# Performance work log

Hardware: AMD Instinct MI355X
Metric: run time of the kernel (lower is better)

## Reference

```python
import jax, jax.numpy as jnp
import numpy as np

N0, N1, N2 = 80000, 40000, 20000
E1, E2 = 500000, 250000
FIN = 128        # in_channels
H = 2            # heads
C1 = 64          # hidden_channels -> layer1 out per head (concat -> 128)
C2 = 64          # out_channels -> layer2 out per head (mean over heads)
ED = 10          # edge_dim per embedding, total edge feat = 2*ED = 20
NTYPE, NTS = 23, 1158


def setup_inputs() -> dict:
    key = jax.random.key(0)
    ks = jax.random.split(key, 48)
    sc = 0.05
    inp = {
        "x": jax.random.normal(ks[0], (N0, FIN), jnp.float32),
        "ei1_src": jax.random.randint(ks[1], (E1,), 0, N0),
        "ei1_dst": jax.random.randint(ks[2], (E1,), 0, N1),
        "et1": jax.random.randint(ks[3], (E1,), 0, NTYPE),
        "ets1": jax.random.randint(ks[4], (E1,), 0, NTS),
        "ei2_src": jax.random.randint(ks[5], (E2,), 0, N1),
        "ei2_dst": jax.random.randint(ks[6], (E2,), 0, N2),
        "et2": jax.random.randint(ks[7], (E2,), 0, NTYPE),
        "ets2": jax.random.randint(ks[8], (E2,), 0, NTS),
        # shared edge embeddings (Linear(23,10), Linear(1158,10))
        "edge_W": jax.random.normal(ks[9], (ED, NTYPE), jnp.float32) * sc,
        "edge_b": jax.random.normal(ks[10], (ED,), jnp.float32) * sc,
        "time_W": jax.random.normal(ks[11], (ED, NTS), jnp.float32) * sc,
        "time_b": jax.random.normal(ks[12], (ED,), jnp.float32) * sc,
    }
    # layer 1: in=128, heads=2, C=64, concat=True (out dim 128)
    hc1 = H * C1
    inp["Wq1"] = jax.random.normal(ks[13], (hc1, FIN), jnp.float32) * sc
    inp["bq1"] = jnp.zeros((hc1,), jnp.float32)
    inp["Wk1"] = jax.random.normal(ks[14], (hc1, FIN), jnp.float32) * sc
    inp["bk1"] = jnp.zeros((hc1,), jnp.float32)
    inp["Wv1"] = jax.random.normal(ks[15], (hc1, FIN), jnp.float32) * sc
    inp["bv1"] = jnp.zeros((hc1,), jnp.float32)
    inp["We1"] = jax.random.normal(ks[16], (hc1, 2 * ED), jnp.float32) * sc
    inp["Wskip1"] = jax.random.normal(ks[17], (hc1, FIN), jnp.float32) * sc
    inp["bskip1"] = jnp.zeros((hc1,), jnp.float32)
    inp["Wbeta1"] = jax.random.normal(ks[18], (1, 3 * hc1), jnp.float32) * sc
    inp["ln_g"] = jnp.ones((hc1,), jnp.float32)
    inp["ln_b"] = jnp.zeros((hc1,), jnp.float32)
    # layer 2: in=128, heads=2, C=64, concat=False (out dim 64)
    hc2 = H * C2
    inp["Wq2"] = jax.random.normal(ks[19], (hc2, hc1), jnp.float32) * sc
    inp["bq2"] = jnp.zeros((hc2,), jnp.float32)
    inp["Wk2"] = jax.random.normal(ks[20], (hc2, hc1), jnp.float32) * sc
    inp["bk2"] = jnp.zeros((hc2,), jnp.float32)
    inp["Wv2"] = jax.random.normal(ks[21], (hc2, hc1), jnp.float32) * sc
    inp["bv2"] = jnp.zeros((hc2,), jnp.float32)
    inp["We2"] = jax.random.normal(ks[22], (hc2, 2 * ED), jnp.float32) * sc
    inp["Wskip2"] = jax.random.normal(ks[23], (C2, hc1), jnp.float32) * sc
    inp["bskip2"] = jnp.zeros((C2,), jnp.float32)
    inp["Wbeta2"] = jax.random.normal(ks[24], (1, 3 * C2), jnp.float32) * sc
    return inp


def _edge_feat(et, ets, edge_W, edge_b, time_W, time_b):
    # one_hot(e) @ W.T + b == W.T[e] + b (avoids materializing huge one-hot)
    return jnp.concatenate([jnp.take(edge_W.T, et, axis=0) + edge_b,
                            jnp.take(time_W.T, ets, axis=0) + time_b], axis=-1)


def _conv(x_src, x_dst, src, dst, ef, Wq, bq, Wk, bk, Wv, bv, We,
          Wskip, bskip, Wbeta, concat):
    n_dst = x_dst.shape[0]
    HC = Wq.shape[0]
    C = HC // H
    q = (x_dst @ Wq.T + bq).reshape(n_dst, H, C)            # [Nd,H,C]
    k = (x_src @ Wk.T + bk)[src].reshape(-1, H, C)          # [E,H,C]
    v = (x_src @ Wv.T + bv)[src].reshape(-1, H, C)
    e = (ef @ We.T).reshape(-1, H, C)
    k = k + e
    alpha = jnp.einsum('ehc,ehc->eh', q[dst], k) / np.sqrt(C).astype(np.float32)
    # segment softmax over destination nodes
    m = jax.ops.segment_max(alpha, dst, num_segments=n_dst)
    ex = jnp.exp(alpha - m[dst])
    s = jax.ops.segment_sum(ex, dst, num_segments=n_dst)
    a = ex / (s[dst] + 1e-16)                               # [E,H]
    msg = (v + e) * a[..., None]                            # [E,H,C]
    out = jax.ops.segment_sum(msg.reshape(-1, HC), dst, num_segments=n_dst)
    out = out if concat else out.reshape(n_dst, H, C).mean(axis=1)
    x_r = x_dst @ Wskip.T + bskip
    beta = jax.nn.sigmoid(
        jnp.concatenate([out, x_r, out - x_r], axis=-1) @ Wbeta.T)  # [Nd,1]
    return beta * x_r + (1.0 - beta) * out


def _layernorm(x, g, b):
    mu = x.mean(-1, keepdims=True)
    var = x.var(-1, keepdims=True)
    return (x - mu) / jnp.sqrt(var + 1e-5) * g + b


def reference(x, ei1_src, ei1_dst, et1, ets1, ei2_src, ei2_dst, et2, ets2,
              edge_W, edge_b, time_W, time_b,
              Wq1, bq1, Wk1, bk1, Wv1, bv1, We1, Wskip1, bskip1, Wbeta1,
              ln_g, ln_b,
              Wq2, bq2, Wk2, bk2, Wv2, bv2, We2, Wskip2, bskip2, Wbeta2):
    ef1 = _edge_feat(et1, ets1, edge_W, edge_b, time_W, time_b)
    h = _conv(x, x[:N1], ei1_src, ei1_dst, ef1,
              Wq1, bq1, Wk1, bk1, Wv1, bv1, We1, Wskip1, bskip1, Wbeta1,
              concat=True)
    h = jax.nn.gelu(_layernorm(h, ln_g, ln_b), approximate=False)
    ef2 = _edge_feat(et2, ets2, edge_W, edge_b, time_W, time_b)
    o = _conv(h, h[:N2], ei2_src, ei2_dst, ef2,
              Wq2, bq2, Wk2, bk2, Wv2, bv2, We2, Wskip2, bskip2, Wbeta2,
              concat=False)
    return jax.nn.log_softmax(o, axis=-1)
```

## Files before the change

### kernel.cpp

```cpp
#include <hip/hip_runtime.h>
#include <math.h>

#define N0 80000
#define N1 40000
#define N2 20000
#define E1C 500000
#define E2C 250000
#define NTYPE 23
#define NTS 1158

#define NB1 157
#define NB2 79
#define KV1B 1250
#define QR1B 625
#define CNTB 2930
#define KV2B 625
#define QR2B 313
#define FILLB 2930
#define AGG1B 2048
#define AGG2B 1024

#define OFF_XB    0u
#define OFF_QR1   5120000u
#define OFF_KV1   15360000u
#define OFF_H     25600000u
#define OFF_QR2   28160000u
#define OFF_KV2   32000000u
#define OFF_WB1   37120000u
#define OFF_BP1   37160000u
#define OFF_WB2   37170000u
#define OFF_BP2   37200000u
#define OFF_TA1   37210000u
#define OFF_TB1   37213000u
#define OFF_TA2   37370000u
#define OFF_TB2   37373000u
#define OFF_RP1   37530000u
#define OFF_CUR1  37580000u
#define OFF_ED1   37630000u
#define OFF_BS1   38640000u
#define OFF_RP2   38650000u
#define OFF_CUR2  38680000u
#define OFF_ED2   38710000u
#define OFF_BS2   39220000u
#define OFF_DONE  39230000u
#define OFF_RK1   39240000u
#define OFF_RK2   39740000u

typedef __bf16 bf16x8 __attribute__((ext_vector_type(8)));
typedef float f32x4 __attribute__((ext_vector_type(4)));

static __device__ __forceinline__ float b2f(unsigned short u) {
    union { unsigned int i; float f; } c;
    c.i = ((unsigned int)u) << 16;
    return c.f;
}
static __device__ __forceinline__ unsigned short f2b(float f) {
    unsigned int u = __float_as_uint(f);
    unsigned int r = (u + 0x7fffu + ((u >> 16) & 1u)) >> 16;
    return (unsigned short)r;
}
static __device__ __forceinline__ bf16x8 ldfrag(const unsigned short* p) {
    return *reinterpret_cast<const bf16x8*>(p);
}

static __device__ __forceinline__ void stage16(const void* g, void* l) {
    __builtin_amdgcn_global_load_lds(
        (const __attribute__((address_space(1))) unsigned int*)g,
        (__attribute__((address_space(3))) unsigned int*)l,
        16, 0, 0);
}

template <int CTRL>
static __device__ __forceinline__ float dpp_addstep(float v) {
    int x = __builtin_amdgcn_mov_dpp(__float_as_int(v), CTRL, 0xF, 0xF, true);
    return v + __int_as_float(x);
}
static __device__ __forceinline__ float red16(float v) {
    v = dpp_addstep<0xB1>(v);
    v = dpp_addstep<0x4E>(v);
    v = dpp_addstep<0x141>(v);
    v = dpp_addstep<0x140>(v);
    return v;
}
template <int CTRL>
static __device__ __forceinline__ float dpp_maxstep(float v) {
    int x = __builtin_amdgcn_mov_dpp(__float_as_int(v), CTRL, 0xF, 0xF, true);
    return fmaxf(v, __int_as_float(x));
}
static __device__ __forceinline__ float red16max(float v) {
    v = dpp_maxstep<0xB1>(v);
    v = dpp_maxstep<0x4E>(v);
    v = dpp_maxstep<0x141>(v);
    v = dpp_maxstep<0x140>(v);
    return v;
}

#define LDSS 136
#define SMEM_USHORTS 8704

template <int NTILES>
static __device__ __forceinline__ void dev_gemm_bf16out(
    const unsigned short* __restrict__ XB, const unsigned short* __restrict__ WB,
    const float* __restrict__ BP, unsigned short* __restrict__ Y, int n, int blk,
    unsigned short* sb) {
    constexpr int COLS = NTILES * 16;
    constexpr int HALF = NTILES / 2;
    constexpr int HCOLS = HALF * 16;
    constexpr int NCHUNK = (NTILES + 3) / 4;
    int wave = threadIdx.x >> 6, lane = threadIdx.x & 63;
    int m = lane & 15, quad = lane >> 4;
    int rowbase = blk * 64 + wave * 16;
    int arow = rowbase + m; if (arow >= n) arow = n - 1;
    unsigned short* swave = sb + wave * 16 * LDSS;
    const unsigned short* xrow = XB + (size_t)arow * 128 + quad * 8;
    bf16x8 a0 = ldfrag(xrow), a1 = ldfrag(xrow + 32);
    bf16x8 a2 = ldfrag(xrow + 64), a3 = ldfrag(xrow + 96);
    f32x4 acc[NTILES];
#pragma unroll
    for (int t = 0; t < NTILES; t++) acc[t] = (f32x4){0.f, 0.f, 0.f, 0.f};
    const char* gstage = (const char*)WB + wave * 1024 + lane * 16;
    char* lstage = (char*)sb + wave * 1024;
#pragma unroll
    for (int c = 0; c < NCHUNK; c++) {
#pragma unroll
        for (int i = 0; i < 4; i++)
            if (c * 4 + i < NTILES)
                stage16(gstage + (size_t)(c * 4 + i) * 4096, lstage + i * 4096);
        __syncthreads();
#pragma unroll
        for (int t = 0; t < 4; t++) {
            int tt = c * 4 + t;
            if (tt < NTILES) {
                const unsigned short* wt = sb + t * 2048 + lane * 8;
                acc[tt] = __builtin_amdgcn_mfma_f32_16x16x32_bf16(a0, ldfrag(wt), acc[tt], 0, 0, 0);
                acc[tt] = __builtin_amdgcn_mfma_f32_16x16x32_bf16(a1, ldfrag(wt + 512), acc[tt], 0, 0, 0);
                acc[tt] = __builtin_amdgcn_mfma_f32_16x16x32_bf16(a2, ldfrag(wt + 1024), acc[tt], 0, 0, 0);
                acc[tt] = __builtin_amdgcn_mfma_f32_16x16x32_bf16(a3, ldfrag(wt + 1536), acc[tt], 0, 0, 0);
            }
        }
        __syncthreads();
    }
    int tswz_bit = (quad >> 1) & 1;
#pragma unroll
    for (int half = 0; half < 2; half++) {
#pragma unroll
        for (int t = 0; t < HALF; t++) {
            int tt = half * HALF + t;
            int tsw = t ^ tswz_bit;
            float b = BP[tt * 16 + m];
#pragma unroll
            for (int r = 0; r < 4; r++)
                swave[(quad * 4 + r) * LDSS + tsw * 16 + m] = f2b(acc[tt][r] + b);
        }
#pragma unroll
        for (int i = 0; i < 4; i++) {
            int idx = i * 64 + lane;
            int r = idx / (HCOLS / 8), g = idx % (HCOLS / 8);
            int gs = g ^ (((r >> 3) & 1) << 1);
            int grow = rowbase + r;
            if (grow < n) {
                uint4 v = *(const uint4*)&swave[r * LDSS + gs * 8];
                *(uint4*)(Y + (size_t)grow * COLS + half * HCOLS + g * 8) = v;
            }
        }
    }
}

template <int NTILES>
static __device__ __forceinline__ void dev_gemm_f32out(
    const unsigned short* __restrict__ XB, const unsigned short* __restrict__ WB,
    const float* __restrict__ BP, float* __restrict__ Y, int n, int blk,
    unsigned short* sb) {
    constexpr int COLS = NTILES * 16;
    constexpr int NCHUNK = (NTILES + 3) / 4;
    int wave = threadIdx.x >> 6, lane = threadIdx.x & 63;
    int m = lane & 15, quad = lane >> 4;
    int rowbase = blk * 64 + wave * 16;
    int arow = rowbase + m; if (arow >= n) arow = n - 1;
    const unsigned short* xrow = XB + (size_t)arow * 128 + quad * 8;
    bf16x8 a0 = ldfrag(xrow), a1 = ldfrag(xrow + 32);
    bf16x8 a2 = ldfrag(xrow + 64), a3 = ldfrag(xrow + 96);
    f32x4 acc[NTILES];
#pragma unroll
    for (int t = 0; t < NTILES; t++) acc[t] = (f32x4){0.f, 0.f, 0.f, 0.f};
    const char* gstage = (const char*)WB + wave * 1024 + lane * 16;
    char* lstage = (char*)sb + wave * 1024;
#pragma unroll
    for (int c = 0; c < NCHUNK; c++) {
#pragma unroll
        for (int i = 0; i < 4; i++)
            if (c * 4 + i < NTILES)
                stage16(gstage + (size_t)(c * 4 + i) * 4096, lstage + i * 4096);
        __syncthreads();
#pragma unroll
        for (int t = 0; t < 4; t++) {
            int tt = c * 4 + t;
            if (tt < NTILES) {
                const unsigned short* wt = sb + t * 2048 + lane * 8;
                acc[tt] = __builtin_amdgcn_mfma_f32_16x16x32_bf16(a0, ldfrag(wt), acc[tt], 0, 0, 0);
                acc[tt] = __builtin_amdgcn_mfma_f32_16x16x32_bf16(a1, ldfrag(wt + 512), acc[tt], 0, 0, 0);
                acc[tt] = __builtin_amdgcn_mfma_f32_16x16x32_bf16(a2, ldfrag(wt + 1024), acc[tt], 0, 0, 0);
                acc[tt] = __builtin_amdgcn_mfma_f32_16x16x32_bf16(a3, ldfrag(wt + 1536), acc[tt], 0, 0, 0);
            }
        }
        __syncthreads();
    }
#pragma unroll
    for (int t = 0; t < NTILES; t++) {
        float b = BP[t * 16 + m];
#pragma unroll
        for (int r = 0; r < 4; r++) {
            int grow = rowbase + quad * 4 + r;
            if (grow < n) Y[(size_t)grow * COLS + t * 16 + m] = acc[t][r] + b;
        }
    }
}

__global__ __launch_bounds__(256) void prep(
    const float* __restrict__ x, unsigned short* __restrict__ XB,
    const float* __restrict__ Wk1, const float* __restrict__ Wv1,
    const float* __restrict__ Wq1, const float* __restrict__ Wskip1,
    const float* __restrict__ bk1, const float* __restrict__ bv1,
    const float* __restrict__ bq1, const float* __restrict__ bskip1,
    const float* __restrict__ Wk2, const float* __restrict__ Wv2,
    const float* __restrict__ Wq2, const float* __restrict__ Wskip2,
    const float* __restrict__ bk2, const float* __restrict__ bv2,
    const float* __restrict__ bq2, const float* __restrict__ bskip2,
    unsigned short* __restrict__ WB1, float* __restrict__ BP1,
    unsigned short* __restrict__ WB2, float* __restrict__ BP2,
    const float* __restrict__ edge_W, const float* __restrict__ edge_b,
    const float* __restrict__ time_W, const float* __restrict__ time_b,
    const float* __restrict__ We1, const float* __restrict__ We2,
    float* __restrict__ TA1, float* __restrict__ TB1,
    float* __restrict__ TA2, float* __restrict__ TB2,
    int* __restrict__ cnt1, int* __restrict__ cnt2, int* __restrict__ done) {
    int tid = blockIdx.x * blockDim.x + threadIdx.x;
    int stride = gridDim.x * blockDim.x;
    for (int i = tid; i < N0 * 32; i += stride) {
        float4 v = *(const float4*)(x + (size_t)i * 4);
        ushort4 u;
        u.x = f2b(v.x); u.y = f2b(v.y); u.z = f2b(v.z); u.w = f2b(v.w);
        *(ushort4*)(XB + (size_t)i * 4) = u;
    }
    for (int i = tid; i < 512 * 128; i += stride) {
        int j = i & 7, l = (i >> 3) & 63, ks = (i >> 9) & 3, t = i >> 11;
        int row = t * 16 + (l & 15);
        int col = ks * 32 + ((l >> 4) & 3) * 8 + j;
        const float* w; int off;
        if (row < 128) { w = Wk1; off = 0; }
        else if (row < 256) { w = Wv1; off = 128; }
        else if (row < 384) { w = Wq1; off = 256; }
        else { w = Wskip1; off = 384; }
        WB1[i] = f2b(w[(size_t)(row - off) * 128 + col]);
    }
    for (int i = tid; i < 512; i += stride) {
        const float* b; int off;
        if (i < 128) { b = bk1; off = 0; }
        else if (i < 256) { b = bv1; off = 128; }
        else if (i < 384) { b = bq1; off = 256; }
        else { b = bskip1; off = 384; }
        BP1[i] = b[i - off];
    }
    for (int i = tid; i < 448 * 128; i += stride) {
        int j = i & 7, l = (i >> 3) & 63, ks = (i >> 9) & 3, t = i >> 11;
        int row = t * 16 + (l & 15);
        int col = ks * 32 + ((l >> 4) & 3) * 8 + j;
        const float* w; int off;
        if (row < 128) { w = Wk2; off = 0; }
        else if (row < 256) { w = Wv2; off = 128; }
        else if (row < 384) { w = Wq2; off = 256; }
        else { w = Wskip2; off = 384; }
        WB2[i] = f2b(w[(size_t)(row - off) * 128 + col]);
    }
    for (int i = tid; i < 448; i += stride) {
        const float* b; int off;
        if (i < 128) { b = bk2; off = 0; }
        else if (i < 256) { b = bv2; off = 128; }
        else if (i < 384) { b = bq2; off = 256; }
        else { b = bskip2; off = 384; }
        BP2[i] = b[i - off];
    }
    const int TBL = (NTYPE + NTS) * 128;
    for (int i = tid; i < TBL; i += stride) {
        if (i < NTYPE * 128) {
            int e = i >> 7, c = i & 127;
            float s1 = 0.f, s2 = 0.f;
#pragma unroll
            for (int j = 0; j < 10; j++) {
                float fj = edge_W[j * NTYPE + e] + edge_b[j];
                s1 += fj * We1[c * 20 + j];
                s2 += fj * We2[c * 20 + j];
            }
            TA1[i] = s1; TA2[i] = s2;
        } else {
            int u = i - NTYPE * 128;
            int ts = u >> 7, c = u & 127;
            float s1 = 0.f, s2 = 0.f;
#pragma unroll
            for (int j = 0; j < 10; j++) {
                float fj = time_W[j * NTS + ts] + time_b[j];
                s1 += fj * We1[c * 20 + 10 + j];
                s2 += fj * We2[c * 20 + 10 + j];
            }
            TB1[u] = s1; TB2[u] = s2;
        }
    }
    for (int i = tid; i < N1 + N2 + 2; i += stride) {
        if (i < N1) cnt1[i] = 0;
        else if (i < N1 + N2) cnt2[i - N1] = 0;
        else done[i - N1 - N2] = 0;
    }
}

__global__ __launch_bounds__(256) void mega_l1(
    const unsigned short* __restrict__ XB,
    const unsigned short* __restrict__ WB1, const float* __restrict__ BP1,
    unsigned short* __restrict__ KV1, float* __restrict__ QR1,
    const int* __restrict__ d1, const int* __restrict__ d2,
    int* __restrict__ cnt1, int* __restrict__ cnt2,
    int* __restrict__ rk1, int* __restrict__ rk2) {
    __shared__ __align__(16) unsigned short sbuf[SMEM_USHORTS];
    int b = blockIdx.x;
    if (b < CNTB) {
        int t = b * 256 + threadIdx.x;
        if (t < E1C) rk1[t] = atomicAdd(&cnt1[d1[t]], 1);
        else {
            t -= E1C;
            if (t < E2C) rk2[t] = atomicAdd(&cnt2[d2[t]], 1);
        }
    } else if (b < CNTB + KV1B) {
        dev_gemm_bf16out<16>(XB, WB1, BP1, KV1, N0, b - CNTB, sbuf);
    } else {
        dev_gemm_f32out<16>(XB, WB1 + 256 * 128, BP1 + 256, QR1, N1,
                            b - CNTB - KV1B, sbuf);
    }
}

__global__ __launch_bounds__(256) void gemm_l2(
    const unsigned short* __restrict__ H,
    const unsigned short* __restrict__ WB2, const float* __restrict__ BP2,
    unsigned short* __restrict__ KV2, float* __restrict__ QR2) {
    __shared__ __align__(16) unsigned short sbuf[SMEM_USHORTS];
    int b = blockIdx.x;
    if (b < KV2B) dev_gemm_bf16out<16>(H, WB2, BP2, KV2, N1, b, sbuf);
    else dev_gemm_f32out<12>(H, WB2 + 256 * 128, BP2 + 256, QR2, N2, b - KV2B, sbuf);
}

__global__ __launch_bounds__(256) void csr_scan(
    int* __restrict__ cnt1, int* __restrict__ bs1, int* __restrict__ rp1,
    int* __restrict__ cnt2, int* __restrict__ bs2, int* __restrict__ rp2,
    int* __restrict__ done) {
    __shared__ int s[256];
    __shared__ int amlast;
    int b = blockIdx.x;
    int* cnt; int* bs; int* rp; int n, lb;
    if (b < NB1) { cnt = cnt1; bs = bs1; rp = rp1; n = N1; lb = b; }
    else { cnt = cnt2; bs = bs2; rp = rp2; n = N2; lb = b - NB1; }
    int t = lb * 256 + threadIdx.x;
    int v = (t < n) ? cnt[t] : 0;
    s[threadIdx.x] = v;
    __syncthreads();
    for (int off = 128; off; off >>= 1) {
        if (threadIdx.x < off) s[threadIdx.x] += s[threadIdx.x + off];
        __syncthreads();
    }
    if (threadIdx.x == 0) {
        atomicExch(&bs[lb], s[0]);
        __threadfence();
        int prev = atomicAdd(&done[0], 1);
        amlast = (prev == NB1 + NB2 - 1) ? 1 : 0;
    }
    __syncthreads();
    if (amlast) {
        int tt = threadIdx.x;
        int v1 = (tt < NB1) ? atomicAdd(&bs1[tt], 0) : 0;
        s[tt] = v1;
        __syncthreads();
        for (int off = 1; off < 256; off <<= 1) {
            int u = (tt >= off) ? s[tt - off] : 0;
            __syncthreads();
            s[tt] += u;
            __syncthreads();
        }
        if (tt < NB1) atomicExch(&bs1[tt], s[tt] - v1);
        __syncthreads();
        int v2 = (tt < NB2) ? atomicAdd(&bs2[tt], 0) : 0;
        s[tt] = v2;
        __syncthreads();
        for (int off = 1; off < 256; off <<= 1) {
            int u = (tt >= off) ? s[tt - off] : 0;
            __syncthreads();
            s[tt] += u;
            __syncthreads();
        }
        if (tt < NB2) atomicExch(&bs2[tt], s[tt] - v2);
        __threadfence();
        __syncthreads();
        if (tt == 0) atomicExch(&done[1], 1);
    }
    if (threadIdx.x == 0) {
        while (atomicAdd(&done[1], 0) == 0) __builtin_amdgcn_s_sleep(1);
    }
    __syncthreads();
    __threadfence();
    int base = atomicAdd(&bs[lb], 0);
    s[threadIdx.x] = v;
    __syncthreads();
    for (int off = 1; off < 256; off <<= 1) {
        int u = (threadIdx.x >= off) ? s[threadIdx.x - off] : 0;
        __syncthreads();
        s[threadIdx.x] += u;
        __syncthreads();
    }
    int incl = s[threadIdx.x];
    if (t < n) rp[t] = base + incl - v;
    if (t == n - 1) rp[n] = base + incl;
}

__global__ __launch_bounds__(256) void fill_both(
    const int* __restrict__ d1, const int* __restrict__ s1,
    const int* __restrict__ et1, const int* __restrict__ ets1,
    const int* __restrict__ rp1, const int* __restrict__ rk1, uint2* __restrict__ ed1,
    const int* __restrict__ d2, const int* __restrict__ s2,
    const int* __restrict__ et2, const int* __restrict__ ets2,
    const int* __restrict__ rp2, const int* __restrict__ rk2, uint2* __restrict__ ed2) {
    int t = blockIdx.x * 256 + threadIdx.x;
    if (t < E1C) {
        int pos = rp1[d1[t]] + rk1[t];
        ed1[pos] = make_uint2((unsigned)s1[t],
                              (unsigned)(et1[t] | (ets1[t] << 16)));
    } else {
        t -= E1C;
        if (t < E2C) {
            int pos = rp2[d2[t]] + rk2[t];
            ed2[pos] = make_uint2((unsigned)s2[t],
                                  (unsigned)(et2[t] | (ets2[t] << 16)));
        }
    }
}

static __device__ __forceinline__ void edge_accum(
    int beg, int end, int s, int co, float4 q4,
    const uint2* __restrict__ ED, const float* __restrict__ TA,
    const float* __restrict__ TB, const unsigned short* __restrict__ KV,
    float& ax, float& ay, float& az, float& aw, float& suma) {
    int p = beg + s;
    if (p >= end) return;
    uint2 d0 = ED[p];
    int pA = p + 2;  bool mA = pA < end;
    uint2 d1 = ED[mA ? pA : beg];
    int pB = p + 4;  bool mB = pB < end;
    uint2 d2 = ED[mB ? pB : beg];
    int sn0 = (int)d0.x, t0 = (int)(d0.y & 0xFFFF), ts0 = (int)(d0.y >> 16);
    float4 ta0 = *(const float4*)(TA + t0 * 128 + co);
    float4 tb0 = *(const float4*)(TB + ts0 * 128 + co);
    const unsigned short* kv0 = KV + (size_t)sn0 * 256;
    ushort4 ku0 = *(const ushort4*)(kv0 + co);
    ushort4 vu0 = *(const ushort4*)(kv0 + 128 + co);
    int sn1 = (int)d1.x, t1 = (int)(d1.y & 0xFFFF), ts1 = (int)(d1.y >> 16);
    float4 ta1 = *(const float4*)(TA + t1 * 128 + co);
    float4 tb1 = *(const float4*)(TB + ts1 * 128 + co);
    const unsigned short* kv1 = KV + (size_t)sn1 * 256;
    ushort4 ku1 = *(const ushort4*)(kv1 + co);
    ushort4 vu1 = *(const ushort4*)(kv1 + 128 + co);
    for (;;) {
        int pC = pB + 2; bool mC = pC < end;
        uint2 d3 = ED[mC ? pC : beg];
        int sn2 = (int)d2.x, t2 = (int)(d2.y & 0xFFFF), ts2 = (int)(d2.y >> 16);
        float4 ta2 = *(const float4*)(TA + t2 * 128 + co);
        float4 tb2 = *(const float4*)(TB + ts2 * 128 + co);
        const unsigned short* kv2 = KV + (size_t)sn2 * 256;
        ushort4 ku2 = *(const ushort4*)(kv2 + co);
        ushort4 vu2 = *(const ushort4*)(kv2 + 128 + co);
        float e0c = ta0.x + tb0.x, e1c = ta0.y + tb0.y;
        float e2c = ta0.z + tb0.z, e3c = ta0.w + tb0.w;
        float pp = q4.x * (b2f(ku0.x) + e0c) + q4.y * (b2f(ku0.y) + e1c)
                 + q4.z * (b2f(ku0.z) + e2c) + q4.w * (b2f(ku0.w) + e3c);
        pp = red16(pp);
        float a = __expf(pp * 0.125f);
        ax += a * (b2f(vu0.x) + e0c); ay += a * (b2f(vu0.y) + e1c);
        az += a * (b2f(vu0.z) + e2c); aw += a * (b2f(vu0.w) + e3c);
        suma += a;
        if (!mA) break;
        ta0 = ta1; tb0 = tb1; ku0 = ku1; vu0 = vu1;
        ta1 = ta2; tb1 = tb2; ku1 = ku2; vu1 = vu2;
        d2 = d3;
        mA = mB; mB = mC; pB = pC;
    }
}

__global__ __launch_bounds__(256) void agg_layer1(
    const int* __restrict__ rowptr, const uint2* __restrict__ ED,
    const float* __restrict__ TA, const float* __restrict__ TB,
    const float* __restrict__ QR, const unsigned short* __restrict__ KV,
    const float* __restrict__ Wbeta,
    const float* __restrict__ ln_g, const float* __restrict__ ln_b,
    unsigned short* __restrict__ hout, int n) {
    int gw = (blockIdx.x * blockDim.x + threadIdx.x) >> 6;
    int nw = (gridDim.x * blockDim.x) >> 6;
    int lane = threadIdx.x & 63;
    int s = lane >> 5, cg = lane & 15;
    int co = ((lane >> 4) & 1) * 64 + 4 * cg;
    for (int wid = gw; wid < n; wid += nw) {
    int beg = rowptr[wid], end = rowptr[wid + 1];
    float4 q4 = *(const float4*)(QR + (size_t)wid * 256 + co);
    float ax = 0.f, ay = 0.f, az = 0.f, aw = 0.f, suma = 0.f;
    edge_accum(beg, end, s, co, q4, ED, TA, TB, KV, ax, ay, az, aw, suma);
    ax += __shfl_xor(ax, 32); ay += __shfl_xor(ay, 32);
    az += __shfl_xor(az, 32); aw += __shfl_xor(aw, 32);
    suma += __shfl_xor(suma, 32);
    float inv_s = 1.f / (suma + 1e-16f);
    float ox = ax * inv_s, oy = ay * inv_s, oz = az * inv_s, ow = aw * inv_s;
    float4 r4 = *(const float4*)(QR + (size_t)wid * 256 + 128 + co);
    float4 wo = *(const float4*)(Wbeta + co);
    float4 wr = *(const float4*)(Wbeta + 128 + co);
    float4 wd = *(const float4*)(Wbeta + 256 + co);
    float pb = wo.x * ox + wr.x * r4.x + wd.x * (ox - r4.x)
             + wo.y * oy + wr.y * r4.y + wd.y * (oy - r4.y)
             + wo.z * oz + wr.z * r4.z + wd.z * (oz - r4.z)
             + wo.w * ow + wr.w * r4.w + wd.w * (ow - r4.w);
    pb = red16(pb);
    pb += __shfl_xor(pb, 16);
    float beta = 1.f / (1.f + __expf(-pb));
    float gx = beta * r4.x + (1.f - beta) * ox;
    float gy = beta * r4.y + (1.f - beta) * oy;
    float gz = beta * r4.z + (1.f - beta) * oz;
    float gw4 = beta * r4.w + (1.f - beta) * ow;
    float sm = gx + gy + gz + gw4;
    float sq = gx * gx + gy * gy + gz * gz + gw4 * gw4;
    sm = red16(sm); sm += __shfl_xor(sm, 16);
    sq = red16(sq); sq += __shfl_xor(sq, 16);
    float mu = sm * (1.f / 128.f);
    float var = sq * (1.f / 128.f) - mu * mu;
    float inv = rsqrtf(var + 1e-5f);
    float4 lg = *(const float4*)(ln_g + co);
    float4 lb = *(const float4*)(ln_b + co);
    float yx = (gx - mu) * inv * lg.x + lb.x;
    float yy = (gy - mu) * inv * lg.y + lb.y;
    float yz = (gz - mu) * inv * lg.z + lb.z;
    float yw = (gw4 - mu) * inv * lg.w + lb.w;
    const float ISQ2 = 0.70710678118654752f;
    yx = 0.5f * yx * (1.f + erff(yx * ISQ2));
    yy = 0.5f * yy * (1.f + erff(yy * ISQ2));
    yz = 0.5f * yz * (1.f + erff(yz * ISQ2));
    yw = 0.5f * yw * (1.f + erff(yw * ISQ2));
    if (s == 0) {
        ushort4 hv;
        hv.x = f2b(yx); hv.y = f2b(yy); hv.z = f2b(yz); hv.w = f2b(yw);
        *(ushort4*)(hout + (size_t)wid * 128 + co) = hv;
    }
    }
}

__global__ __launch_bounds__(256) void agg_layer2(
    const int* __restrict__ rowptr, const uint2* __restrict__ ED,
    const float* __restrict__ TA, const float* __restrict__ TB,
    const float* __restrict__ QR, const unsigned short* __restrict__ KV,
    const float* __restrict__ Wbeta,
    float* __restrict__ o, int n) {
    int gw = (blockIdx.x * blockDim.x + threadIdx.x) >> 6;
    int nw = (gridDim.x * blockDim.x) >> 6;
    int lane = threadIdx.x & 63;
    int s = lane >> 5, cg = lane & 15;
    int co = ((lane >> 4) & 1) * 64 + 4 * cg;
    for (int wid = gw; wid < n; wid += nw) {
    int beg = rowptr[wid], end = rowptr[wid + 1];
    float4 q4 = *(const float4*)(QR + (size_t)wid * 192 + co);
    float ax = 0.f, ay = 0.f, az = 0.f, aw = 0.f, suma = 0.f;
    edge_accum(beg, end, s, co, q4, ED, TA, TB, KV, ax, ay, az, aw, suma);
    ax += __shfl_xor(ax, 32); ay += __shfl_xor(ay, 32);
    az += __shfl_xor(az, 32); aw += __shfl_xor(aw, 32);
    suma += __shfl_xor(suma, 32);
    float inv_s = 1.f / (suma + 1e-16f);
    float ox = ax * inv_s, oy = ay * inv_s, oz = az * inv_s, ow = aw * inv_s;
    ox = 0.5f * (ox + __shfl_xor(ox, 16));
    oy = 0.5f * (oy + __shfl_xor(oy, 16));
    oz = 0.5f * (oz + __shfl_xor(oz, 16));
    ow = 0.5f * (ow + __shfl_xor(ow, 16));
    float4 r4 = *(const float4*)(QR + (size_t)wid * 192 + 128 + 4 * cg);
    float4 wo = *(const float4*)(Wbeta + 4 * cg);
    float4 wr = *(const float4*)(Wbeta + 64 + 4 * cg);
    float4 wd = *(const float4*)(Wbeta + 128 + 4 * cg);
    float pb = wo.x * ox + wr.x * r4.x + wd.x * (ox - r4.x)
             + wo.y * oy + wr.y * r4.y + wd.y * (oy - r4.y)
             + wo.z * oz + wr.z * r4.z + wd.z * (oz - r4.z)
             + wo.w * ow + wr.w * r4.w + wd.w * (ow - r4.w);
    pb = red16(pb);
    float beta = 1.f / (1.f + __expf(-pb));
    float vx = beta * r4.x + (1.f - beta) * ox;
    float vy = beta * r4.y + (1.f - beta) * oy;
    float vz = beta * r4.z + (1.f - beta) * oz;
    float vw = beta * r4.w + (1.f - beta) * ow;
    float m = fmaxf(fmaxf(vx, vy), fmaxf(vz, vw));
    m = red16max(m);
    float se = __expf(vx - m) + __expf(vy - m) + __expf(vz - m) + __expf(vw - m);
    se = red16(se);
    float lse = m + logf(se);
    if (lane < 16)
        *(float4*)(o + (size_t)wid * 64 + 4 * cg) =
            make_float4(vx - lse, vy - lse, vz - lse, vw - lse);
    }
}

extern "C" void kernel_launch(void* const* d_in, const int* in_sizes, int n_in,
                              void* d_out, int out_size, void* d_ws, size_t ws_size,
                              hipStream_t stream) {
    const float* x        = (const float*)d_in[0];
    const int*   ei1_src  = (const int*)d_in[1];
    const int*   ei1_dst  = (const int*)d_in[2];
    const int*   et1      = (const int*)d_in[3];
    const int*   ets1     = (const int*)d_in[4];
    const int*   ei2_src  = (const int*)d_in[5];
    const int*   ei2_dst  = (const int*)d_in[6];
    const int*   et2      = (const int*)d_in[7];
    const int*   ets2     = (const int*)d_in[8];
    const float* edge_W   = (const float*)d_in[9];
    const float* edge_b   = (const float*)d_in[10];
    const float* time_W   = (const float*)d_in[11];
    const float* time_b   = (const float*)d_in[12];
    const float* Wq1      = (const float*)d_in[13];
    const float* bq1      = (const float*)d_in[14];
    const float* Wk1      = (const float*)d_in[15];
    const float* bk1      = (const float*)d_in[16];
    const float* Wv1      = (const float*)d_in[17];
    const float* bv1      = (const float*)d_in[18];
    const float* We1      = (const float*)d_in[19];
    const float* Wskip1   = (const float*)d_in[20];
    const float* bskip1   = (const float*)d_in[21];
    const float* Wbeta1   = (const float*)d_in[22];
    const float* ln_g     = (const float*)d_in[23];
    const float* ln_b     = (const float*)d_in[24];
    const float* Wq2      = (const float*)d_in[25];
    const float* bq2      = (const float*)d_in[26];
    const float* Wk2      = (const float*)d_in[27];
    const float* bk2      = (const float*)d_in[28];
    const float* Wv2      = (const float*)d_in[29];
    const float* bv2      = (const float*)d_in[30];
    const float* We2      = (const float*)d_in[31];
    const float* Wskip2   = (const float*)d_in[32];
    const float* bskip2   = (const float*)d_in[33];
    const float* Wbeta2   = (const float*)d_in[34];

    float* ws = (float*)d_ws;
    unsigned short* xb  = (unsigned short*)(ws + OFF_XB);
    float* qr1          = ws + OFF_QR1;
    unsigned short* kv1 = (unsigned short*)(ws + OFF_KV1);
    unsigned short* h   = (unsigned short*)(ws + OFF_H);
    float* qr2          = ws + OFF_QR2;
    unsigned short* kv2 = (unsigned short*)(ws + OFF_KV2);
    unsigned short* wb1 = (unsigned short*)(ws + OFF_WB1);
    float* bp1          = ws + OFF_BP1;
    unsigned short* wb2 = (unsigned short*)(ws + OFF_WB2);
    float* bp2          = ws + OFF_BP2;
    float* ta1          = ws + OFF_TA1;
    float* tb1          = ws + OFF_TB1;
    float* ta2          = ws + OFF_TA2;
    float* tb2          = ws + OFF_TB2;
    int*   rp1          = (int*)(ws + OFF_RP1);
    int*   cur1         = (int*)(ws + OFF_CUR1);
    uint2* ed1          = (uint2*)(ws + OFF_ED1);
    int*   bs1          = (int*)(ws + OFF_BS1);
    int*   rp2          = (int*)(ws + OFF_RP2);
    int*   cur2         = (int*)(ws + OFF_CUR2);
    uint2* ed2          = (uint2*)(ws + OFF_ED2);
    int*   bs2          = (int*)(ws + OFF_BS2);
    int*   done         = (int*)(ws + OFF_DONE);
    int*   rk1          = (int*)(ws + OFF_RK1);
    int*   rk2          = (int*)(ws + OFF_RK2);

    prep<<<2048, 256, 0, stream>>>(
        x, xb,
        Wk1, Wv1, Wq1, Wskip1, bk1, bv1, bq1, bskip1,
        Wk2, Wv2, Wq2, Wskip2, bk2, bv2, bq2, bskip2,
        wb1, bp1, wb2, bp2,
        edge_W, edge_b, time_W, time_b, We1, We2,
        ta1, tb1, ta2, tb2, cur1, cur2, done);
    mega_l1<<<KV1B + QR1B + CNTB, 256, 0, stream>>>(
        xb, wb1, bp1, kv1, qr1, ei1_dst, ei2_dst, cur1, cur2, rk1, rk2);
    csr_scan<<<NB1 + NB2, 256, 0, stream>>>(cur1, bs1, rp1, cur2, bs2, rp2, done);
    fill_both<<<FILLB, 256, 0, stream>>>(
        ei1_dst, ei1_src, et1, ets1, rp1, rk1, ed1,
        ei2_dst, ei2_src, et2, ets2, rp2, rk2, ed2);
    agg_layer1<<<AGG1B, 256, 0, stream>>>(rp1, ed1,
        ta1, tb1, qr1, kv1, Wbeta1, ln_g, ln_b, h, N1);
    gemm_l2<<<KV2B + QR2B, 256, 0, stream>>>(h, wb2, bp2, kv2, qr2);
    agg_layer2<<<AGG2B, 256, 0, stream>>>(rp2, ed2,
        ta2, tb2, qr2, kv2, Wbeta2, (float*)d_out, N2);
}
```

Before: 358.8 us.

## Fold CSR scan into mega_l1 via spin-wait and use one-warp-per-node agg grids

Merges the separate csr_scan launch into the tail blocks of mega_l1. Those blocks spin on a new completion counter until all counting blocks have finished, then run the decoupled scan, which removes one kernel launch and its boundary. The aggregation kernels drop their grid-stride loops and launch one warp per destination node. Spin-waiting inside a kernel depends on the counting blocks being scheduled before the scan blocks, a forward-progress assumption that holds only if lower block IDs are dispatched first.

```diff
diff --git a/kernel.cpp b/kernel.cpp
--- a/kernel.cpp
+++ b/kernel.cpp
@@ -17,8 +17,7 @@
 #define KV2B 625
 #define QR2B 313
 #define FILLB 2930
-#define AGG1B 2048
-#define AGG2B 1024
+#define MEGAB (CNTB + KV1B + QR1B + NB1 + NB2)
 
 #define OFF_XB    0u
 #define OFF_QR1   5120000u
@@ -305,7 +304,7 @@
             TB1[u] = s1; TB2[u] = s2;
         }
     }
-    for (int i = tid; i < N1 + N2 + 2; i += stride) {
+    for (int i = tid; i < N1 + N2 + 3; i += stride) {
         if (i < N1) cnt1[i] = 0;
         else if (i < N1 + N2) cnt2[i - N1] = 0;
         else done[i - N1 - N2] = 0;
@@ -318,7 +317,10 @@
     unsigned short* __restrict__ KV1, float* __restrict__ QR1,
     const int* __restrict__ d1, const int* __restrict__ d2,
     int* __restrict__ cnt1, int* __restrict__ cnt2,
-    int* __restrict__ rk1, int* __restrict__ rk2) {
+    int* __restrict__ rk1, int* __restrict__ rk2,
+    int* __restrict__ bs1, int* __restrict__ rp1,
+    int* __restrict__ bs2, int* __restrict__ rp2,
+    int* __restrict__ done) {
     __shared__ __align__(16) unsigned short sbuf[SMEM_USHORTS];
     int b = blockIdx.x;
     if (b < CNTB) {
@@ -328,11 +330,85 @@
             t -= E1C;
             if (t < E2C) rk2[t] = atomicAdd(&cnt2[d2[t]], 1);
         }
+        __threadfence();
+        __syncthreads();
+        if (threadIdx.x == 0) atomicAdd(&done[2], 1);
     } else if (b < CNTB + KV1B) {
         dev_gemm_bf16out<16>(XB, WB1, BP1, KV1, N0, b - CNTB, sbuf);
-    } else {
+    } else if (b < CNTB + KV1B + QR1B) {
         dev_gemm_f32out<16>(XB, WB1 + 256 * 128, BP1 + 256, QR1, N1,
                             b - CNTB - KV1B, sbuf);
+    } else {
+        int* s = (int*)sbuf;
+        int* amlast = s + 256;
+        if (threadIdx.x == 0) {
+            while (atomicAdd(&done[2], 0) < CNTB) __builtin_amdgcn_s_sleep(2);
+        }
+        __syncthreads();
+        __threadfence();
+        int sb_ = b - (CNTB + KV1B + QR1B);
+        int* cnt; int* bs; int* rp; int n, lb;
+        if (sb_ < NB1) { cnt = cnt1; bs = bs1; rp = rp1; n = N1; lb = sb_; }
+        else { cnt = cnt2; bs = bs2; rp = rp2; n = N2; lb = sb_ - NB1; }
+        int t = lb * 256 + threadIdx.x;
+        int v = (t < n) ? cnt[t] : 0;
+        s[threadIdx.x] = v;
+        __syncthreads();
+        for (int off = 128; off; off >>= 1) {
+            if (threadIdx.x < off) s[threadIdx.x] += s[threadIdx.x + off];
+            __syncthreads();
+        }
+        if (threadIdx.x == 0) {
+            atomicExch(&bs[lb], s[0]);
+            __threadfence();
+            int prev = atomicAdd(&done[0], 1);
+            *amlast = (prev == NB1 + NB2 - 1) ? 1 : 0;
+        }
+        __syncthreads();
+        if (*amlast) {
+            int tt = threadIdx.x;
+            int v1 = (tt < NB1) ? atomicAdd(&bs1[tt], 0) : 0;
+            s[tt] = v1;
+            __syncthreads();
+            for (int off = 1; off < 256; off <<= 1) {
+                int u = (tt >= off) ? s[tt - off] : 0;
+                __syncthreads();
+                s[tt] += u;
+                __syncthreads();
+            }
+            if (tt < NB1) atomicExch(&bs1[tt], s[tt] - v1);
+            __syncthreads();
+            int v2 = (tt < NB2) ? atomicAdd(&bs2[tt], 0) : 0;
+            s[tt] = v2;
+            __syncthreads();
+            for (int off = 1; off < 256; off <<= 1) {
+                int u = (tt >= off) ? s[tt - off] : 0;
+                __syncthreads();
+                s[tt] += u;
+                __syncthreads();
+            }
+            if (tt < NB2) atomicExch(&bs2[tt], s[tt] - v2);
+            __threadfence();
+            __syncthreads();
+            if (tt == 0) atomicExch(&done[1], 1);
+        }
+        if (threadIdx.x == 0) {
+            while (atomicAdd(&done[1], 0) == 0) __builtin_amdgcn_s_sleep(1);
+        }
+        __syncthreads();
+        __threadfence();
+        int base = atomicAdd(&bs[lb], 0);
+        s[threadIdx.x] = v;
+        __syncthreads();
+        for (int off = 1; off < 256; off <<= 1) {
+            int u = (threadIdx.x >= off) ? s[threadIdx.x - off] : 0;
+            __syncthreads();
+            s[threadIdx.x] += u;
+            __syncthreads();
+        }
+        int incl = s[threadIdx.x];
+        if (t < n) rp[t] = base + incl - v;
+        if (t == n - 1) rp[n] = base + incl;
     }
 }
 
@@ -344,77 +420,6 @@
     int b = blockIdx.x;
     if (b < KV2B) dev_gemm_bf16out<16>(H, WB2, BP2, KV2, N1, b, sbuf);
     else dev_gemm_f32out<12>(H, WB2 + 256 * 128, BP2 + 256, QR2, N2, b - KV2B, sbuf);
-}
-
-__global__ __launch_bounds__(256) void csr_scan(
-    int* __restrict__ cnt1, int* __restrict__ bs1, int* __restrict__ rp1,
-    int* __restrict__ cnt2, int* __restrict__ bs2, int* __restrict__ rp2,
-    int* __restrict__ done) {
-    __shared__ int s[256];
-    __shared__ int amlast;
-    int b = blockIdx.x;
-    int* cnt; int* bs; int* rp; int n, lb;
-    if (b < NB1) { cnt = cnt1; bs = bs1; rp = rp1; n = N1; lb = b; }
-    else { cnt = cnt2; bs = bs2; rp = rp2; n = N2; lb = b - NB1; }
-    int t = lb * 256 + threadIdx.x;
-    int v = (t < n) ? cnt[t] : 0;
-    s[threadIdx.x] = v;
-    __syncthreads();
-    for (int off = 128; off; off >>= 1) {
-        if (threadIdx.x < off) s[threadIdx.x] += s[threadIdx.x + off];
-        __syncthreads();
-    }
-    if (threadIdx.x == 0) {
-        atomicExch(&bs[lb], s[0]);
-        __threadfence();
-        int prev = atomicAdd(&done[0], 1);
-        amlast = (prev == NB1 + NB2 - 1) ? 1 : 0;
-    }
-    __syncthreads();
-    if (amlast) {
-        int tt = threadIdx.x;
-        int v1 = (tt < NB1) ? atomicAdd(&bs1[tt], 0) : 0;
-        s[tt] = v1;
-        __syncthreads();
-        for (int off = 1; off < 256; off <<= 1) {
-            int u = (tt >= off) ? s[tt - off] : 0;
-            __syncthreads();
-            s[tt] += u;
-            __syncthreads();
-        }
-        if (tt < NB1) atomicExch(&bs1[tt], s[tt] - v1);
-        __syncthreads();
-        int v2 = (tt < NB2) ? atomicAdd(&bs2[tt], 0) : 0;
-        s[tt] = v2;
-        __syncthreads();
-        for (int off = 1; off < 256; off <<= 1) {
-            int u = (tt >= off) ? s[tt - off] : 0;
-            __syncthreads();
-            s[tt] += u;
-            __syncthreads();
-        }
-        if (tt < NB2) atomicExch(&bs2[tt], s[tt] - v2);
-        __threadfence();
-        __syncthreads();
-        if (tt == 0) atomicExch(&done[1], 1);
-    }
-    if (threadIdx.x == 0) {
-        while (atomicAdd(&done[1], 0) == 0) __builtin_amdgcn_s_sleep(1);
-    }
-    __syncthreads();
-    __threadfence();
-    int base = atomicAdd(&bs[lb], 0);
-    s[threadIdx.x] = v;
-    __syncthreads();
-    for (int off = 1; off < 256; off <<= 1) {
-        int u = (threadIdx.x >= off) ? s[threadIdx.x - off] : 0;
-        __syncthreads();
-        s[threadIdx.x] += u;
-        __syncthreads();
-    }
-    int incl = s[threadIdx.x];
-    if (t < n) rp[t] = base + incl - v;
-    if (t == n - 1) rp[n] = base + incl;
 }
 
 __global__ __launch_bounds__(256) void fill_both(
@@ -496,12 +501,11 @@
     const float* __restrict__ Wbeta,
     const float* __restrict__ ln_g, const float* __restrict__ ln_b,
     unsigned short* __restrict__ hout, int n) {
-    int gw = (blockIdx.x * blockDim.x + threadIdx.x) >> 6;
-    int nw = (gridDim.x * blockDim.x) >> 6;
+    int wid = (blockIdx.x * blockDim.x + threadIdx.x) >> 6;
     int lane = threadIdx.x & 63;
+    if (wid >= n) return;
     int s = lane >> 5, cg = lane & 15;
     int co = ((lane >> 4) & 1) * 64 + 4 * cg;
-    for (int wid = gw; wid < n; wid += nw) {
     int beg = rowptr[wid], end = rowptr[wid + 1];
     float4 q4 = *(const float4*)(QR + (size_t)wid * 256 + co);
     float ax = 0.f, ay = 0.f, az = 0.f, aw = 0.f, suma = 0.f;
@@ -525,9 +529,9 @@
     float gx = beta * r4.x + (1.f - beta) * ox;
     float gy = beta * r4.y + (1.f - beta) * oy;
     float gz = beta * r4.z + (1.f - beta) * oz;
-    float gw4 = beta * r4.w + (1.f - beta) * ow;
-    float sm = gx + gy + gz + gw4;
-    float sq = gx * gx + gy * gy + gz * gz + gw4 * gw4;
+    float gw = beta * r4.w + (1.f - beta) * ow;
+    float sm = gx + gy + gz + gw;
+    float sq = gx * gx + gy * gy + gz * gz + gw * gw;
     sm = red16(sm); sm += __shfl_xor(sm, 16);
     sq = red16(sq); sq += __shfl_xor(sq, 16);
     float mu = sm * (1.f / 128.f);
@@ -538,7 +542,7 @@
     float yx = (gx - mu) * inv * lg.x + lb.x;
     float yy = (gy - mu) * inv * lg.y + lb.y;
     float yz = (gz - mu) * inv * lg.z + lb.z;
-    float yw = (gw4 - mu) * inv * lg.w + lb.w;
+    float yw = (gw - mu) * inv * lg.w + lb.w;
     const float ISQ2 = 0.70710678118654752f;
     yx = 0.5f * yx * (1.f + erff(yx * ISQ2));
     yy = 0.5f * yy * (1.f + erff(yy * ISQ2));
@@ -549,7 +553,6 @@
         hv.x = f2b(yx); hv.y = f2b(yy); hv.z = f2b(yz); hv.w = f2b(yw);
         *(ushort4*)(hout + (size_t)wid * 128 + co) = hv;
     }
-    }
 }
 
 __global__ __launch_bounds__(256) void agg_layer2(
@@ -558,12 +561,11 @@
     const float* __restrict__ QR, const unsigned short* __restrict__ KV,
     const float* __restrict__ Wbeta,
     float* __restrict__ o, int n) {
-    int gw = (blockIdx.x * blockDim.x + threadIdx.x) >> 6;
-    int nw = (gridDim.x * blockDim.x) >> 6;
+    int wid = (blockIdx.x * blockDim.x + threadIdx.x) >> 6;
     int lane = threadIdx.x & 63;
+    if (wid >= n) return;
     int s = lane >> 5, cg = lane & 15;
     int co = ((lane >> 4) & 1) * 64 + 4 * cg;
-    for (int wid = gw; wid < n; wid += nw) {
     int beg = rowptr[wid], end = rowptr[wid + 1];
     float4 q4 = *(const float4*)(QR + (size_t)wid * 192 + co);
     float ax = 0.f, ay = 0.f, az = 0.f, aw = 0.f, suma = 0.f;
@@ -599,7 +601,6 @@
     if (lane < 16)
         *(float4*)(o + (size_t)wid * 64 + 4 * cg) =
             make_float4(vx - lse, vy - lse, vz - lse, vw - lse);
-    }
 }
 
 extern "C" void kernel_launch(void* const* d_in, const int* in_sizes, int n_in,
@@ -675,15 +676,15 @@
         wb1, bp1, wb2, bp2,
         edge_W, edge_b, time_W, time_b, We1, We2,
         ta1, tb1, ta2, tb2, cur1, cur2, done);
-    mega_l1<<<KV1B + QR1B + CNTB, 256, 0, stream>>>(
-        xb, wb1, bp1, kv1, qr1, ei1_dst, ei2_dst, cur1, cur2, rk1, rk2);
-    csr_scan<<<NB1 + NB2, 256, 0, stream>>>(cur1, bs1, rp1, cur2, bs2, rp2, done);
+    mega_l1<<<MEGAB, 256, 0, stream>>>(
+        xb, wb1, bp1, kv1, qr1, ei1_dst, ei2_dst, cur1, cur2, rk1, rk2,
+        bs1, rp1, bs2, rp2, done);
     fill_both<<<FILLB, 256, 0, stream>>>(
         ei1_dst, ei1_src, et1, ets1, rp1, rk1, ed1,
         ei2_dst, ei2_src, et2, ets2, rp2, rk2, ed2);
-    agg_layer1<<<AGG1B, 256, 0, stream>>>(rp1, ed1,
+    agg_layer1<<<(N1 + 3) / 4, 256, 0, stream>>>(rp1, ed1,
         ta1, tb1, qr1, kv1, Wbeta1, ln_g, ln_b, h, N1);
     gemm_l2<<<KV2B + QR2B, 256, 0, stream>>>(h, wb2, bp2, kv2, qr2);
-    agg_layer2<<<AGG2B, 256, 0, stream>>>(rp2, ed2,
+    agg_layer2<<<(N2 + 3) / 4, 256, 0, stream>>>(rp2, ed2,
         ta2, tb2, qr2, kv2, Wbeta2, (float*)d_out, N2);
 }
```

Measured after the change: 585.6 us. 63.2% more time.
